# Kernel tuning notes

Measured on AMD Instinct MI355X. Metric: run time of the kernel, lower is better.

The kernel has to match this reference:

```python
import jax, jax.numpy as jnp
import numpy as np

IN_C = 1
BASE_C = 16
N3, N2, N1 = 262144, 65536, 16384

def _quadconv(feat, neigh, w, b):
    # feat: [N, C]; neigh: [N, 9] with -1 padding -> gather via extra zero row
    N = feat.shape[0]
    feat_p = jnp.concatenate([feat, jnp.zeros((1, feat.shape[1]), feat.dtype)], axis=0)
    gidx = jnp.where(neigh == -1, N, neigh)
    col = feat_p[gidx].reshape(N, -1)  # [N, 9*C] im2col
    return col @ w.T + b

def _parent_idx(keys, parent_keys):
    return jnp.searchsorted(parent_keys, keys >> 2)

def _quadpool(feat, keys, parent_keys):
    pidx = _parent_idx(keys, parent_keys)
    p = jax.ops.segment_max(feat, pidx, num_segments=parent_keys.shape[0])
    # original inits with -1e9 and zeroes untouched slots; segment_max uses -inf fill
    return jnp.where(jnp.isneginf(p), jnp.zeros((), feat.dtype), p), pidx

def _quadunpool(feat, keys, parent_keys):
    return feat[_parent_idx(keys, parent_keys)]

def _lin(key, out_f, in_f, scale=0.05):
    kw, kb = jax.random.split(key)
    return (jax.random.normal(kw, (out_f, in_f), jnp.float32) * scale,
            jnp.zeros((out_f,), jnp.float32))

def setup_inputs() -> dict:
    key = jax.random.key(0)
    ks = jax.random.split(key, 12)
    inp = {
        'features': jax.random.normal(ks[0], (N3, IN_C), jnp.float32),
        'keys3': jnp.arange(N3, dtype=jnp.int32),
        'keys2': jnp.arange(N2, dtype=jnp.int32),
        'keys1': jnp.arange(N1, dtype=jnp.int32),
        'neighs3': jax.random.randint(ks[1], (N3, 9), -1, N3, jnp.int32),
        'neighs2': jax.random.randint(ks[2], (N2, 9), -1, N2, jnp.int32),
        'neighs1': jax.random.randint(ks[3], (N1, 9), -1, N1, jnp.int32),
    }
    c = BASE_C
    inp['w_enc1'], inp['b_enc1'] = _lin(ks[4], c, 9 * IN_C)
    inp['w_enc2'], inp['b_enc2'] = _lin(ks[5], 2 * c, 9 * c)
    inp['w_enc3'], inp['b_enc3'] = _lin(ks[6], 4 * c, 9 * 2 * c)
    inp['w_dec1'], inp['b_dec1'] = _lin(ks[7], 2 * c, 9 * 4 * c)
    inp['w_dec2'], inp['b_dec2'] = _lin(ks[8], c, 9 * 2 * c)
    inp['w_head'], inp['b_head'] = _lin(ks[9], IN_C, 9 * c)
    return inp

def reference(features, keys3, keys2, keys1, neighs3, neighs2, neighs1,
              w_enc1, b_enc1, w_enc2, b_enc2, w_enc3, b_enc3,
              w_dec1, b_dec1, w_dec2, b_dec2, w_head, b_head):
    relu = jax.nn.relu
    x8 = relu(_quadconv(features, neighs3, w_enc1, b_enc1))
    x7_p, _ = _quadpool(x8, keys3, keys2)
    x7 = relu(_quadconv(x7_p, neighs2, w_enc2, b_enc2))
    x6_p, _ = _quadpool(x7, keys2, keys1)
    x6 = relu(_quadconv(x6_p, neighs1, w_enc3, b_enc3))
    x7_up = _quadunpool(x6, keys2, keys1)
    x7_dec = relu(_quadconv(x7_up, neighs2, w_dec1, b_dec1))
    x8_up = _quadunpool(x7_dec, keys3, keys2)
    x8_dec = relu(_quadconv(x8_up, neighs3, w_dec2, b_dec2))
    return _quadconv(x8_dec, neighs3, w_head, b_head)
```

## Files before the change

### kernel.cpp

```cpp
#include <hip/hip_runtime.h>
#include <stdint.h>

#define NN3 262144
#define NN2 65536
#define NN1 16384

typedef __attribute__((ext_vector_type(8))) __bf16 bf16x8;
typedef __attribute__((ext_vector_type(4))) float floatx4;

static __device__ __forceinline__ float bf2f(unsigned short u) {
    union { unsigned int i; float f; } v; v.i = ((unsigned int)u) << 16; return v.f;
}
static __device__ __forceinline__ unsigned short f2bf(float f) {
    union { float f; unsigned int i; } v; v.f = f;
    unsigned int x = v.i;
    return (unsigned short)((x + 0x7fffu + ((x >> 16) & 1u)) >> 16);
}
static __device__ __forceinline__ bf16x8 zero_bf16x8() {
    bf16x8 z;
#pragma unroll
    for (int i = 0; i < 8; ++i) z[i] = (__bf16)0.0f;
    return z;
}

__global__ __launch_bounds__(256) void enc1pool_kernel(
    const float* __restrict__ feat, const int* __restrict__ neigh,
    const float* __restrict__ w, const float* __restrict__ b,
    unsigned short* __restrict__ x7p,
    const float* __restrict__ w_enc2, const float* __restrict__ w_enc3,
    const float* __restrict__ w_dec1, const float* __restrict__ w_dec2,
    unsigned short* __restrict__ wb_enc2, unsigned short* __restrict__ wb_enc3,
    unsigned short* __restrict__ wb_dec1, unsigned short* __restrict__ wb_dec2)
{
    {
        int g = blockIdx.x * 256 + threadIdx.x;
        if (g < 4608) wb_enc2[g] = f2bf(w_enc2[g]);
        else {
            g -= 4608;
            if (g < 18432) wb_enc3[g] = f2bf(w_enc3[g]);
            else {
                g -= 18432;
                if (g < 18432) wb_dec1[g] = f2bf(w_dec1[g]);
                else { g -= 18432; if (g < 4608) wb_dec2[g] = f2bf(w_dec2[g]); }
            }
        }
    }
    __shared__ float ws[144];
    __shared__ float bs[16];
    __shared__ int nsh[2304];
    int t = threadIdx.x;
    if (t < 144) ws[t] = w[t];
    if (t < 16)  bs[t] = b[t];
    int base = blockIdx.x * 256;
    for (int e = t; e < 2304; e += 256) nsh[e] = neigh[(size_t)base * 9 + e];
    __syncthreads();
    float f[9];
#pragma unroll
    for (int k = 0; k < 9; ++k) { int j = nsh[t * 9 + k]; f[k] = (j < 0) ? 0.0f : feat[j]; }
    float v[16];
#pragma unroll
    for (int co = 0; co < 16; ++co) {
        float a = bs[co];
#pragma unroll
        for (int k = 0; k < 9; ++k) a += f[k] * ws[co * 9 + k];
        v[co] = fmaxf(a, 0.0f);
    }
#pragma unroll
    for (int co = 0; co < 16; ++co) {
        v[co] = fmaxf(v[co], __shfl_xor(v[co], 1));
        v[co] = fmaxf(v[co], __shfl_xor(v[co], 2));
    }
    if ((t & 3) == 0) {
        unsigned int ov[8];
#pragma unroll
        for (int h = 0; h < 8; ++h)
            ov[h] = (unsigned int)f2bf(v[2 * h]) | (((unsigned int)f2bf(v[2 * h + 1])) << 16);
        uint4* dst = (uint4*)(x7p + (size_t)((base + t) >> 2) * 16);
        dst[0] = make_uint4(ov[0], ov[1], ov[2], ov[3]);
        dst[1] = make_uint4(ov[4], ov[5], ov[6], ov[7]);
    }
}

template <int CIN, int COUT, bool SHIFT, bool POOL>
__global__ __launch_bounds__(256) void conv_mfma(
    const unsigned short* __restrict__ src, const int* __restrict__ neigh,
    const unsigned short* __restrict__ wb, const float* __restrict__ bias,
    unsigned short* __restrict__ dst)
{
    constexpr int K  = 9 * CIN;
    constexpr int KT = (K + 31) / 32;
    constexpr int NT = COUT / 16;
    __shared__ int nsh[576];
    int t = threadIdx.x;
    int rowbase = blockIdx.x * 64;
    for (int e = t; e < 576; e += 256) {
        int j = neigh[(size_t)rowbase * 9 + e];
        if (SHIFT) j = (j < 0) ? -1 : (j >> 2);
        nsh[e] = j;
    }
    __syncthreads();
    int lane = t & 63;
    int wave = t >> 6;
    int m    = lane & 15;
    int quad = lane >> 4;
    int mrow = wave * 16 + m;
    floatx4 acc[NT];
#pragma unroll
    for (int n = 0; n < NT; ++n) acc[n] = (floatx4){0.f, 0.f, 0.f, 0.f};
#pragma unroll
    for (int kt = 0; kt < KT; ++kt) {
        int k0 = kt * 32 + quad * 8;
        bf16x8 a = zero_bf16x8();
        if (k0 < K) {
            int nb = k0 / CIN;
            int ci = k0 % CIN;
            int j  = nsh[mrow * 9 + nb];
            if (j >= 0) a = *(const bf16x8*)(src + (size_t)j * CIN + ci);
        }
#pragma unroll
        for (int n = 0; n < NT; ++n) {
            bf16x8 bfrag = zero_bf16x8();
            if (k0 < K) bfrag = *(const bf16x8*)(wb + (size_t)(n * 16 + m) * K + k0);
            acc[n] = __builtin_amdgcn_mfma_f32_16x16x32_bf16(a, bfrag, acc[n], 0, 0, 0);
        }
    }
    if (POOL) {
        int p = (rowbase >> 2) + wave * 4 + quad;
#pragma unroll
        for (int n = 0; n < NT; ++n) {
            int cout = n * 16 + m;
            float vm = fmaxf(fmaxf(acc[n][0], acc[n][1]), fmaxf(acc[n][2], acc[n][3]));
            float v  = fmaxf(vm + bias[cout], 0.0f);
            dst[(size_t)p * COUT + cout] = f2bf(v);
        }
    } else {
        int grow = rowbase + wave * 16 + quad * 4;
#pragma unroll
        for (int n = 0; n < NT; ++n) {
            int cout = n * 16 + m;
            float bv = bias[cout];
#pragma unroll
            for (int r = 0; r < 4; ++r) {
                float v = fmaxf(acc[n][r] + bv, 0.0f);
                dst[(size_t)(grow + r) * COUT + cout] = f2bf(v);
            }
        }
    }
}

static __device__ __forceinline__ float dot2(unsigned int u, const float* w) {
    return bf2f((unsigned short)(u & 0xffffu)) * w[0] + bf2f((unsigned short)(u >> 16)) * w[1];
}
__global__ __launch_bounds__(256) void head_kernel(
    const unsigned short* __restrict__ x, const int* __restrict__ neigh,
    const float* __restrict__ w, const float* __restrict__ b, float* __restrict__ out)
{
    __shared__ float ws[144];
    __shared__ int nsh[2304];
    int t = threadIdx.x;
    if (t < 144) ws[t] = w[t];
    int base = blockIdx.x * 256;
    for (int e = t; e < 2304; e += 256) nsh[e] = neigh[(size_t)base * 9 + e];
    __syncthreads();
    float acc = b[0];
#pragma unroll
    for (int k = 0; k < 9; ++k) {
        int j = nsh[t * 9 + k];
        if (j >= 0) {
            const uint4* r = (const uint4*)(x + (size_t)j * 16);
            uint4 r0 = r[0], r1 = r[1];
            const float* wp = &ws[k * 16];
            acc += dot2(r0.x, wp)     + dot2(r0.y, wp + 2)  + dot2(r0.z, wp + 4)  + dot2(r0.w, wp + 6);
            acc += dot2(r1.x, wp + 8) + dot2(r1.y, wp + 10) + dot2(r1.z, wp + 12) + dot2(r1.w, wp + 14);
        }
    }
    out[base + t] = acc;
}

extern "C" void kernel_launch(void* const* d_in, const int* in_sizes, int n_in,
                              void* d_out, int out_size, void* d_ws, size_t ws_size,
                              hipStream_t stream) {
    const float* features = (const float*)d_in[0];
    const int* neighs3 = (const int*)d_in[4];
    const int* neighs2 = (const int*)d_in[5];
    const int* neighs1 = (const int*)d_in[6];
    const float* w_enc1 = (const float*)d_in[7];
    const float* b_enc1 = (const float*)d_in[8];
    const float* w_enc2 = (const float*)d_in[9];
    const float* b_enc2 = (const float*)d_in[10];
    const float* w_enc3 = (const float*)d_in[11];
    const float* b_enc3 = (const float*)d_in[12];
    const float* w_dec1 = (const float*)d_in[13];
    const float* b_dec1 = (const float*)d_in[14];
    const float* w_dec2 = (const float*)d_in[15];
    const float* b_dec2 = (const float*)d_in[16];
    const float* w_head = (const float*)d_in[17];
    const float* b_head = (const float*)d_in[18];

    char* ws = (char*)d_ws;
    size_t off = 0;
    unsigned short* wb_enc2 = (unsigned short*)(ws + off); off += 4608 * 2;
    unsigned short* wb_enc3 = (unsigned short*)(ws + off); off += 18432 * 2;
    unsigned short* wb_dec1 = (unsigned short*)(ws + off); off += 18432 * 2;
    unsigned short* wb_dec2 = (unsigned short*)(ws + off); off += 4608 * 2;
    unsigned short* x7p   = (unsigned short*)(ws + off); off += (size_t)NN2 * 16 * 2;
    unsigned short* x6p   = (unsigned short*)(ws + off); off += (size_t)NN1 * 32 * 2;
    unsigned short* x6    = (unsigned short*)(ws + off); off += (size_t)NN1 * 64 * 2;
    unsigned short* x7dec = (unsigned short*)(ws + off); off += (size_t)NN2 * 32 * 2;
    unsigned short* x8dec = (unsigned short*)(ws + off); off += (size_t)NN3 * 16 * 2;

    enc1pool_kernel<<<NN3 / 256, 256, 0, stream>>>(features, neighs3, w_enc1, b_enc1, x7p,
                                                   w_enc2, w_enc3, w_dec1, w_dec2,
                                                   wb_enc2, wb_enc3, wb_dec1, wb_dec2);
    conv_mfma<16, 32, false, true><<<NN2 / 64, 256, 0, stream>>>(x7p, neighs2, wb_enc2, b_enc2, x6p);
    conv_mfma<32, 64, false, false><<<NN1 / 64, 256, 0, stream>>>(x6p, neighs1, wb_enc3, b_enc3, x6);
    conv_mfma<64, 32, true, false><<<NN2 / 64, 256, 0, stream>>>(x6, neighs2, wb_dec1, b_dec1, x7dec);
    conv_mfma<32, 16, true, false><<<NN3 / 64, 256, 0, stream>>>(x7dec, neighs3, wb_dec2, b_dec2, x8dec);
    head_kernel<<<NN3 / 256, 256, 0, stream>>>(x8dec, neighs3, w_head, b_head, (float*)d_out);
}
```

Measured before the change: 203.8 us.

## Process multiple row tiles per block in MFMA convs and head, use nontemporal neighbor loads

Adds a TILES template parameter so each conv block handles several 64-row tiles, reusing each loaded weight fragment across tiles and issuing more independent gathers per wave. The head kernel now computes two outputs per thread, and neighbor-index loads and output stores use nontemporal hints. The goal is to amortize weight loads and index setup and to raise memory-level parallelism. The cost is fewer blocks, more registers and shared memory per block, and the kt loop is no longer forced to unroll, which could reduce occupancy or ILP.

After: 202.2 us. About the same (-0.8%).

```diff
diff --git a/kernel.cpp b/kernel.cpp
--- a/kernel.cpp
+++ b/kernel.cpp
@@ -52,7 +52,8 @@
     if (t < 144) ws[t] = w[t];
     if (t < 16)  bs[t] = b[t];
     int base = blockIdx.x * 256;
-    for (int e = t; e < 2304; e += 256) nsh[e] = neigh[(size_t)base * 9 + e];
+    for (int e = t; e < 2304; e += 256)
+        nsh[e] = __builtin_nontemporal_load(&neigh[(size_t)base * 9 + e]);
     __syncthreads();
     float f[9];
 #pragma unroll
@@ -81,7 +82,7 @@
     }
 }
 
-template <int CIN, int COUT, bool SHIFT, bool POOL>
+template <int CIN, int COUT, bool SHIFT, bool POOL, int TILES>
 __global__ __launch_bounds__(256) void conv_mfma(
     const unsigned short* __restrict__ src, const int* __restrict__ neigh,
     const unsigned short* __restrict__ wb, const float* __restrict__ bias,
@@ -90,11 +91,11 @@
     constexpr int K  = 9 * CIN;
     constexpr int KT = (K + 31) / 32;
     constexpr int NT = COUT / 16;
-    __shared__ int nsh[576];
+    __shared__ int nsh[576 * TILES];
     int t = threadIdx.x;
-    int rowbase = blockIdx.x * 64;
-    for (int e = t; e < 576; e += 256) {
-        int j = neigh[(size_t)rowbase * 9 + e];
+    int rowbase = blockIdx.x * (64 * TILES);
+    for (int e = t; e < 576 * TILES; e += 256) {
+        int j = __builtin_nontemporal_load(&neigh[(size_t)rowbase * 9 + e]);
         if (SHIFT) j = (j < 0) ? -1 : (j >> 2);
         nsh[e] = j;
     }
@@ -103,46 +104,57 @@
     int wave = t >> 6;
     int m    = lane & 15;
     int quad = lane >> 4;
-    int mrow = wave * 16 + m;
-    floatx4 acc[NT];
-#pragma unroll
-    for (int n = 0; n < NT; ++n) acc[n] = (floatx4){0.f, 0.f, 0.f, 0.f};
-#pragma unroll
+    int mrow9 = (wave * 16 + m) * 9;
+    floatx4 acc[TILES][NT];
+#pragma unroll
+    for (int tl = 0; tl < TILES; ++tl)
+#pragma unroll
+        for (int n = 0; n < NT; ++n) acc[tl][n] = (floatx4){0.f, 0.f, 0.f, 0.f};
     for (int kt = 0; kt < KT; ++kt) {
         int k0 = kt * 32 + quad * 8;
-        bf16x8 a = zero_bf16x8();
-        if (k0 < K) {
-            int nb = k0 / CIN;
-            int ci = k0 % CIN;
-            int j  = nsh[mrow * 9 + nb];
-            if (j >= 0) a = *(const bf16x8*)(src + (size_t)j * CIN + ci);
+        bf16x8 a[TILES];
+#pragma unroll
+        for (int tl = 0; tl < TILES; ++tl) {
+            a[tl] = zero_bf16x8();
+            if (k0 < K) {
+                int nb = k0 / CIN;
+                int ci = k0 % CIN;
+                int j  = nsh[tl * 576 + mrow9 + nb];
+                if (j >= 0) a[tl] = *(const bf16x8*)(src + (size_t)j * CIN + ci);
+            }
         }
 #pragma unroll
         for (int n = 0; n < NT; ++n) {
             bf16x8 bfrag = zero_bf16x8();
             if (k0 < K) bfrag = *(const bf16x8*)(wb + (size_t)(n * 16 + m) * K + k0);
-            acc[n] = __builtin_amdgcn_mfma_f32_16x16x32_bf16(a, bfrag, acc[n], 0, 0, 0);
-        }
-    }
-    if (POOL) {
-        int p = (rowbase >> 2) + wave * 4 + quad;
-#pragma unroll
-        for (int n = 0; n < NT; ++n) {
-            int cout = n * 16 + m;
-            float vm = fmaxf(fmaxf(acc[n][0], acc[n][1]), fmaxf(acc[n][2], acc[n][3]));
-            float v  = fmaxf(vm + bias[cout], 0.0f);
-            dst[(size_t)p * COUT + cout] = f2bf(v);
-        }
-    } else {
-        int grow = rowbase + wave * 16 + quad * 4;
-#pragma unroll
-        for (int n = 0; n < NT; ++n) {
-            int cout = n * 16 + m;
-            float bv = bias[cout];
-#pragma unroll
-            for (int r = 0; r < 4; ++r) {
-                float v = fmaxf(acc[n][r] + bv, 0.0f);
-                dst[(size_t)(grow + r) * COUT + cout] = f2bf(v);
+#pragma unroll
+            for (int tl = 0; tl < TILES; ++tl)
+                acc[tl][n] = __builtin_amdgcn_mfma_f32_16x16x32_bf16(a[tl], bfrag, acc[tl][n], 0, 0, 0);
+        }
+    }
+#pragma unroll
+    for (int tl = 0; tl < TILES; ++tl) {
+        int tbase = rowbase + tl * 64;
+        if (POOL) {
+            int p = (tbase >> 2) + wave * 4 + quad;
+#pragma unroll
+            for (int n = 0; n < NT; ++n) {
+                int cout = n * 16 + m;
+                float vm = fmaxf(fmaxf(acc[tl][n][0], acc[tl][n][1]), fmaxf(acc[tl][n][2], acc[tl][n][3]));
+                float v  = fmaxf(vm + bias[cout], 0.0f);
+                dst[(size_t)p * COUT + cout] = f2bf(v);
+            }
+        } else {
+            int grow = tbase + wave * 16 + quad * 4;
+#pragma unroll
+            for (int n = 0; n < NT; ++n) {
+                int cout = n * 16 + m;
+                float bv = bias[cout];
+#pragma unroll
+                for (int r = 0; r < 4; ++r) {
+                    float v = fmaxf(acc[tl][n][r] + bv, 0.0f);
+                    dst[(size_t)(grow + r) * COUT + cout] = f2bf(v);
+                }
             }
         }
     }
@@ -156,25 +168,34 @@
     const float* __restrict__ w, const float* __restrict__ b, float* __restrict__ out)
 {
     __shared__ float ws[144];
-    __shared__ int nsh[2304];
+    __shared__ int nsh[4608];
     int t = threadIdx.x;
     if (t < 144) ws[t] = w[t];
-    int base = blockIdx.x * 256;
-    for (int e = t; e < 2304; e += 256) nsh[e] = neigh[(size_t)base * 9 + e];
+    int base = blockIdx.x * 512;
+    for (int e = t; e < 4608; e += 256)
+        nsh[e] = __builtin_nontemporal_load(&neigh[(size_t)base * 9 + e]);
     __syncthreads();
-    float acc = b[0];
+    float acc0 = b[0], acc1 = b[0];
 #pragma unroll
     for (int k = 0; k < 9; ++k) {
-        int j = nsh[t * 9 + k];
-        if (j >= 0) {
-            const uint4* r = (const uint4*)(x + (size_t)j * 16);
+        int j0 = nsh[t * 9 + k];
+        int j1 = nsh[(256 + t) * 9 + k];
+        const float* wp = &ws[k * 16];
+        if (j0 >= 0) {
+            const uint4* r = (const uint4*)(x + (size_t)j0 * 16);
             uint4 r0 = r[0], r1 = r[1];
-            const float* wp = &ws[k * 16];
-            acc += dot2(r0.x, wp)     + dot2(r0.y, wp + 2)  + dot2(r0.z, wp + 4)  + dot2(r0.w, wp + 6);
-            acc += dot2(r1.x, wp + 8) + dot2(r1.y, wp + 10) + dot2(r1.z, wp + 12) + dot2(r1.w, wp + 14);
-        }
-    }
-    out[base + t] = acc;
+            acc0 += dot2(r0.x, wp)     + dot2(r0.y, wp + 2)  + dot2(r0.z, wp + 4)  + dot2(r0.w, wp + 6);
+            acc0 += dot2(r1.x, wp + 8) + dot2(r1.y, wp + 10) + dot2(r1.z, wp + 12) + dot2(r1.w, wp + 14);
+        }
+        if (j1 >= 0) {
+            const uint4* r = (const uint4*)(x + (size_t)j1 * 16);
+            uint4 r0 = r[0], r1 = r[1];
+            acc1 += dot2(r0.x, wp)     + dot2(r0.y, wp + 2)  + dot2(r0.z, wp + 4)  + dot2(r0.w, wp + 6);
+            acc1 += dot2(r1.x, wp + 8) + dot2(r1.y, wp + 10) + dot2(r1.z, wp + 12) + dot2(r1.w, wp + 14);
+        }
+    }
+    __builtin_nontemporal_store(acc0, &out[base + t]);
+    __builtin_nontemporal_store(acc1, &out[base + 256 + t]);
 }
 
 extern "C" void kernel_launch(void* const* d_in, const int* in_sizes, int n_in,
@@ -212,9 +233,9 @@
     enc1pool_kernel<<<NN3 / 256, 256, 0, stream>>>(features, neighs3, w_enc1, b_enc1, x7p,
                                                    w_enc2, w_enc3, w_dec1, w_dec2,
                                                    wb_enc2, wb_enc3, wb_dec1, wb_dec2);
-    conv_mfma<16, 32, false, true><<<NN2 / 64, 256, 0, stream>>>(x7p, neighs2, wb_enc2, b_enc2, x6p);
-    conv_mfma<32, 64, false, false><<<NN1 / 64, 256, 0, stream>>>(x6p, neighs1, wb_enc3, b_enc3, x6);
-    conv_mfma<64, 32, true, false><<<NN2 / 64, 256, 0, stream>>>(x6, neighs2, wb_dec1, b_dec1, x7dec);
-    conv_mfma<32, 16, true, false><<<NN3 / 64, 256, 0, stream>>>(x7dec, neighs3, wb_dec2, b_dec2, x8dec);
-    head_kernel<<<NN3 / 256, 256, 0, stream>>>(x8dec, neighs3, w_head, b_head, (float*)d_out);
-}
+    conv_mfma<16, 32, false, true, 2><<<NN2 / 128, 256, 0, stream>>>(x7p, neighs2, wb_enc2, b_enc2, x6p);
+    conv_mfma<32, 64, false, false, 1><<<NN1 / 64, 256, 0, stream>>>(x6p, neighs1, wb_enc3, b_enc3, x6);
+    conv_mfma<64, 32, true, false, 2><<<NN2 / 128, 256, 0, stream>>>(x6, neighs2, wb_dec1, b_dec1, x7dec);
+    conv_mfma<32, 16, true, false, 4><<<NN3 / 256, 256, 0, stream>>>(x7dec, neighs3, wb_dec2, b_dec2, x8dec);
+    head_kernel<<<NN3 / 512, 256, 0, stream>>>(x8dec, neighs3, w_head, b_head, (float*)d_out);
+}
```
